# Kernel tuning notes

Hardware: AMD Instinct MI355X
Metric: run time of the kernel (lower is better)

## Reference

```python
import jax, jax.numpy as jnp
import numpy as np

N_NODES = 100000
N_EDGES = 3200000
D_FEAT = 64
CLAMP = 20.0
POSINF = 1.0e6
NEGINF = -1.0e6


def setup_inputs() -> dict:
    key = jax.random.key(0)
    k1, k2, k3, k4 = jax.random.split(key, 4)
    x = jax.random.normal(k1, (N_NODES, D_FEAT), dtype=jnp.float32)
    edge_src = jax.random.randint(k2, (N_EDGES,), 0, N_NODES, dtype=jnp.int64 if jax.config.jax_enable_x64 else jnp.int32).astype(jnp.int32)
    edge_dst = jax.random.randint(k3, (N_EDGES,), 0, N_NODES, dtype=jnp.int32)
    # symmetric-normalized-adjacency-like positive weights
    edge_w = jax.random.uniform(k4, (N_EDGES,), dtype=jnp.float32)
    t = jnp.zeros((1,), dtype=jnp.float32)
    return {"t": t, "x": x, "edge_src": edge_src, "edge_dst": edge_dst, "edge_w": edge_w}


def reference(t, x, edge_src, edge_dst, edge_w):
    # out = sparse.mm(G, x): out[dst] += w * x[src]  (COO SpMM via segment_sum)
    msgs = edge_w[:, None] * x[edge_src]                 # [E, d]
    out = jax.ops.segment_sum(msgs, edge_dst, num_segments=N_NODES)  # [N, d]
    # numerical_stability epilogue: nan/inf sanitize + clamp
    out = jnp.nan_to_num(out, nan=0.0, posinf=POSINF, neginf=NEGINF)
    out = jnp.clip(out, -CLAMP, CLAMP)
    return out
```

## Files before the change

### kernel.cpp

```cpp
#include <hip/hip_runtime.h>
#include <hip/hip_fp16.h>
#include <math.h>

#define N_NODES 100000
#define N_EDGES 3200000
#define D_FEAT  64
#define CLAMP_V 20.0f

#define BSH 6
#define BSZ 64
#define NB  1563
#define SBNSH 11
#define NSB 49
#define FPS 32
#define CPAD 32
#define CHUNKP 4096
#define NCHUNK ((N_EDGES + CHUNKP - 1) / CHUNKP)
#define CH2 4096
#define SLICES 16
#define CAPL 2560
#define HISTB 512
#define NSLC 4
#define NBIN 256


__global__ __launch_bounds__(256)
void prep_kernel(const float4* __restrict__ xin, ushort4* __restrict__ xh,
                 const int* __restrict__ edst, int* __restrict__ counts,
                 int n4) {
    __shared__ int h[NB];
    if (blockIdx.x < HISTB) {
        for (int i = threadIdx.x; i < NB; i += blockDim.x) h[i] = 0;
        __syncthreads();
        const int4* d4p = (const int4*)edst;
        int total4 = N_EDGES >> 2;
        for (int i = blockIdx.x * blockDim.x + threadIdx.x; i < total4;
             i += HISTB * blockDim.x) {
            int4 d4 = d4p[i];
            atomicAdd(&h[d4.x >> BSH], 1);
            atomicAdd(&h[d4.y >> BSH], 1);
            atomicAdd(&h[d4.z >> BSH], 1);
            atomicAdd(&h[d4.w >> BSH], 1);
        }
        __syncthreads();
        for (int i = threadIdx.x; i < NB; i += blockDim.x) {
            int v = h[i];
            if (v) atomicAdd(&counts[i * CPAD], v);
        }
    } else {
        int i = (blockIdx.x - HISTB) * blockDim.x + threadIdx.x;
        if (i < n4) {
            float4 v = xin[i];
            ushort4 o;
            o.x = __half_as_ushort(__float2half(v.x));
            o.y = __half_as_ushort(__float2half(v.y));
            o.z = __half_as_ushort(__float2half(v.z));
            o.w = __half_as_ushort(__float2half(v.w));
            xh[i] = o;
        }
    }
}

__global__ void scan_kernel(const int* __restrict__ counts,
                            int* __restrict__ bstarts,
                            int* __restrict__ cursors2,
                            int* __restrict__ cursors1) {
    __shared__ int wsum[16];
    int t = threadIdx.x;
    int lane = t & 63, wv = t >> 6;
    int b0 = t * 2, b1 = t * 2 + 1;
    int c0 = (b0 < NB) ? counts[b0 * CPAD] : 0;
    int c1 = (b1 < NB) ? counts[b1 * CPAD] : 0;
    int v = c0 + c1;
    int sc = v;
#pragma unroll
    for (int off = 1; off < 64; off <<= 1) {
        int u = __shfl_up(sc, off);
        if (lane >= off) sc += u;
    }
    if (lane == 63) wsum[wv] = sc;
    __syncthreads();
    if (wv == 0 && lane < 16) {
        int ws = wsum[lane];
#pragma unroll
        for (int off = 1; off < 16; off <<= 1) {
            int u = __shfl_up(ws, off);
            if (lane >= off) ws += u;
        }
        wsum[lane] = ws;
    }
    __syncthreads();
    int base = (wv > 0) ? wsum[wv - 1] : 0;
    int incl = base + sc;
    int excl = incl - v;
    if (b0 < NB) { bstarts[b0] = excl;      cursors2[b0 * CPAD] = excl; }
    if (b1 < NB) { bstarts[b1] = excl + c0; cursors2[b1 * CPAD] = excl + c0; }
    if (t == 1023) bstarts[NB] = incl;
    __syncthreads();
    if (t < NSB) cursors1[t * CPAD] = bstarts[t * FPS];
}

__global__ __launch_bounds__(512)
void pass1_kernel(const int* __restrict__ esrc,
                  const int* __restrict__ edst,
                  const float* __restrict__ ew,
                  int* __restrict__ cursors1,
                  unsigned* __restrict__ rk32,
                  unsigned short* __restrict__ ra16) {
    __shared__ unsigned       spk[CHUNKP];
    __shared__ unsigned short sax[CHUNKP];
    __shared__ unsigned char  binof[CHUNKP];
    __shared__ int h[NSB];
    __shared__ int hstart[NSB];
    __shared__ int lcur[NSB];
    __shared__ int lbase[NSB];

    int c0   = blockIdx.x * CHUNKP;
    int cend = min(c0 + CHUNKP, N_EDGES);
    int n    = cend - c0;
    int nv   = n >> 2;
    const int4*   d4p = (const int4*)(edst + c0);
    const int4*   s4p = (const int4*)(esrc + c0);
    const float4* w4p = (const float4*)(ew + c0);
    int t = threadIdx.x;

    if (t < NSB) h[t] = 0;
    __syncthreads();
    for (int i = t; i < nv; i += 512) {
        int4 d4 = d4p[i];
        atomicAdd(&h[d4.x >> SBNSH], 1);
        atomicAdd(&h[d4.y >> SBNSH], 1);
        atomicAdd(&h[d4.z >> SBNSH], 1);
        atomicAdd(&h[d4.w >> SBNSH], 1);
    }
    __syncthreads();
    if (t < NSB) {
        int c = h[t];
        int sc = c;
#pragma unroll
        for (int off = 1; off < 64; off <<= 1) {
            int u = __shfl_up(sc, off);
            if (t >= off) sc += u;
        }
        int excl = sc - c;
        hstart[t] = excl;
        lcur[t]   = excl;
        lbase[t]  = c ? atomicAdd(&cursors1[t * CPAD], c) : 0;
    }
    __syncthreads();
    for (int i = t; i < nv; i += 512) {
        int4   d4 = d4p[i];
        int4   s4 = s4p[i];
        float4 w4 = w4p[i];
#define PUT(dd, ss, ww)                                                       \
        {                                                                     \
            int bk  = (dd) >> SBNSH;                                          \
            int pos = atomicAdd(&lcur[bk], 1);                                \
            unsigned hw = __half_as_ushort(__float2half(ww));                 \
            spk[pos] = ((hw & 0xFFFEu) << 16) | (unsigned)(ss);               \
            sax[pos] = (unsigned short)((dd) & 2047);                         \
            binof[pos] = (unsigned char)bk;                                   \
        }
        PUT(d4.x, s4.x, w4.x);
        PUT(d4.y, s4.y, w4.y);
        PUT(d4.z, s4.z, w4.z);
        PUT(d4.w, s4.w, w4.w);
#undef PUT
    }
    __syncthreads();
    for (int i = t; i < n; i += 512) {
        int bk = binof[i];
        int o  = lbase[bk] + (i - hstart[bk]);
        rk32[o] = spk[i];
        ra16[o] = sax[i];
    }
}

__global__ __launch_bounds__(512)
void pass2_kernel(const unsigned* __restrict__ rk32,
                  const unsigned short* __restrict__ ra16,
                  const int* __restrict__ bstarts,
                  int* __restrict__ cursors2,
                  unsigned* __restrict__ pk32,
                  unsigned char* __restrict__ nd8) {
    __shared__ unsigned      spk[CH2];
    __shared__ unsigned char snd[CH2];
    __shared__ unsigned char binof[CH2];
    __shared__ int h[FPS];
    __shared__ int lstart[FPS];
    __shared__ int lcur[FPS];
    __shared__ int gbase[FPS];

    int sb    = blockIdx.y;
    int f0    = sb * FPS;
    int fend  = min(f0 + FPS, NB);
    int sb0   = bstarts[f0];
    int sbend = bstarts[fend];
    int t = threadIdx.x;

    for (int s = sb0 + blockIdx.x * CH2; s < sbend; s += SLICES * CH2) {
        int n = min(sbend - s, CH2);
        if (t < FPS) h[t] = 0;
        __syncthreads();
        for (int i = t; i < n; i += 512)
            atomicAdd(&h[(ra16[s + i] >> 6) & (FPS - 1)], 1);
        __syncthreads();
        if (t < FPS) {
            int c = h[t];
            int sc = c;
#pragma unroll
            for (int off = 1; off < 32; off <<= 1) {
                int u = __shfl_up(sc, off);
                if (t >= off) sc += u;
            }
            int excl = sc - c;
            lstart[t] = excl;
            lcur[t]   = excl;
            gbase[t]  = (c && f0 + t < NB)
                          ? atomicAdd(&cursors2[(f0 + t) * CPAD], c) : 0;
        }
        __syncthreads();
        for (int i = t; i < n; i += 512) {
            unsigned       pk = rk32[s + i];
            unsigned short ax = ra16[s + i];
            int fk  = (ax >> 6) & (FPS - 1);
            int pos = atomicAdd(&lcur[fk], 1);
            spk[pos] = pk;
            snd[pos] = (unsigned char)(ax & 63u);
            binof[pos] = (unsigned char)fk;
        }
        __syncthreads();
        for (int i = t; i < n; i += 512) {
            int fk = binof[i];
            int o  = gbase[fk] + (i - lstart[fk]);
            pk32[o] = spk[i];
            nd8[o]  = snd[i];
        }
        __syncthreads();
    }
}

__global__ __launch_bounds__(512)
void sort_gather_kernel(const __half* __restrict__ xh,
                        const unsigned* __restrict__ pk32,
                        const unsigned char* __restrict__ nd8,
                        const int* __restrict__ bstarts,
                        float* __restrict__ out) {
    __shared__ unsigned sbuf[CAPL];
    __shared__ int h[NBIN + 1];
    __shared__ int cur[NBIN];
    __shared__ int wsum4[4];
    int t    = threadIdx.x;
    int lane = t & 63;
    int wv   = t >> 6;
    int g    = lane >> 4;
    int s    = lane & 15;
    const char* xbase = (const char*)xh + (s << 3);

    int b   = blockIdx.x;
    int beg = bstarts[b];
    int cnt = bstarts[b + 1] - beg;
    if (cnt > CAPL) cnt = CAPL;

    if (t <= NBIN) h[t] = 0;
    __syncthreads();
    for (int e = t; e < cnt; e += 512) {
        unsigned p = pk32[beg + e];
        int bin = (int)(((p >> 15) & 3u) << 6) | (int)nd8[beg + e];
        atomicAdd(&h[bin + 1], 1);
    }
    __syncthreads();
    if (t < NBIN) {
        int sc = h[t + 1];
#pragma unroll
        for (int off = 1; off < 64; off <<= 1) {
            int u = __shfl_up(sc, off);
            if (lane >= off) sc += u;
        }
        if (lane == 63) wsum4[wv] = sc;
        __syncthreads();
        if (t == 0) {
            int r = 0;
#pragma unroll
            for (int j = 0; j < 4; ++j) { int v = wsum4[j]; wsum4[j] = r; r += v; }
        }
        __syncthreads();
        h[t + 1] = sc + wsum4[wv];
    } else {
        __syncthreads();
        __syncthreads();
    }
    __syncthreads();
    if (t < NBIN) cur[t] = h[t];
    __syncthreads();
    for (int e = t; e < cnt; e += 512) {
        unsigned p = pk32[beg + e];
        int bin = (int)(((p >> 15) & 3u) << 6) | (int)nd8[beg + e];
        sbuf[atomicAdd(&cur[bin], 1)] = p;
    }
    __syncthreads();

#define GSTEP(EE, A0, A1, A2, A3)                                            \
    {                                                                        \
        unsigned p = sbuf[(EE) + g];                                         \
        float wf = __half2float(__ushort_as_half(                            \
                       (unsigned short)((p >> 16) & 0xFFFEu)));              \
        const ushort4 xv = *(const ushort4*)(xbase +                         \
                       ((size_t)((p & 0x1FFFFu) << 7)));                     \
        A0 = fmaf(__half2float(__ushort_as_half(xv.x)), wf, A0);             \
        A1 = fmaf(__half2float(__ushort_as_half(xv.y)), wf, A1);             \
        A2 = fmaf(__half2float(__ushort_as_half(xv.z)), wf, A2);             \
        A3 = fmaf(__half2float(__ushort_as_half(xv.w)), wf, A3);             \
    }
#define GSTEPC(EE, S1, A0, A1, A2, A3)                                       \
    {                                                                        \
        int eg = (EE) + g;                                                   \
        unsigned p = sbuf[eg < (S1) ? eg : ((S1) - 1)];                      \
        float wf = (eg < (S1)) ? __half2float(__ushort_as_half(              \
                       (unsigned short)((p >> 16) & 0xFFFEu))) : 0.0f;       \
        const ushort4 xv = *(const ushort4*)(xbase +                         \
                       ((size_t)((p & 0x1FFFFu) << 7)));                     \
        A0 = fmaf(__half2float(__ushort_as_half(xv.x)), wf, A0);             \
        A1 = fmaf(__half2float(__ushort_as_half(xv.y)), wf, A1);             \
        A2 = fmaf(__half2float(__ushort_as_half(xv.z)), wf, A2);             \
        A3 = fmaf(__half2float(__ushort_as_half(xv.w)), wf, A3);             \
    }

    int node0 = b << BSH;
    float ak0[8], ak1[8], ak2[8], ak3[8];
#pragma unroll
    for (int k = 0; k < 8; ++k) { ak0[k] = 0.f; ak1[k] = 0.f; ak2[k] = 0.f; ak3[k] = 0.f; }
    for (int blk = 0; blk < NSLC; ++blk) {
#pragma unroll
        for (int k = 0; k < 8; ++k) {
            int seg = (blk << 6) | ((wv << 3) + k);
            int s0 = h[seg];
            int s1 = h[seg + 1];
            int e = s0;
            for (; e + 8 <= s1; e += 8) {
                GSTEP(e,     ak0[k], ak1[k], ak2[k], ak3[k]);
                GSTEP(e + 4, ak0[k], ak1[k], ak2[k], ak3[k]);
            }
            for (; e + 4 <= s1; e += 4)
                GSTEP(e, ak0[k], ak1[k], ak2[k], ak3[k]);
            if (e < s1)
                GSTEPC(e, s1, ak0[k], ak1[k], ak2[k], ak3[k]);
        }
    }
#pragma unroll
    for (int k = 0; k < 8; ++k) {
        float a0 = ak0[k], a1 = ak1[k], a2 = ak2[k], a3 = ak3[k];
        a0 += __shfl_xor(a0, 16); a0 += __shfl_xor(a0, 32);
        a1 += __shfl_xor(a1, 16); a1 += __shfl_xor(a1, 32);
        a2 += __shfl_xor(a2, 16); a2 += __shfl_xor(a2, 32);
        a3 += __shfl_xor(a3, 16); a3 += __shfl_xor(a3, 32);
        if (isnan(a0)) a0 = 0.0f;
        if (isnan(a1)) a1 = 0.0f;
        if (isnan(a2)) a2 = 0.0f;
        if (isnan(a3)) a3 = 0.0f;
        a0 = fminf(fmaxf(a0, -CLAMP_V), CLAMP_V);
        a1 = fminf(fmaxf(a1, -CLAMP_V), CLAMP_V);
        a2 = fminf(fmaxf(a2, -CLAMP_V), CLAMP_V);
        a3 = fminf(fmaxf(a3, -CLAMP_V), CLAMP_V);
        int node = node0 + (wv << 3) + k;
        if (lane < 16 && node < N_NODES)
            *(float4*)(out + ((size_t)node << 6) + (s << 2)) =
                make_float4(a0, a1, a2, a3);
    }
#undef GSTEP
#undef GSTEPC
}

__global__ void zero_kernel(float4* __restrict__ out, int n4) {
    int i = blockIdx.x * blockDim.x + threadIdx.x;
    if (i < n4) out[i] = make_float4(0.f, 0.f, 0.f, 0.f);
}

__global__ void scatter_kernel(const float* __restrict__ x,
                               const int* __restrict__ esrc,
                               const int* __restrict__ edst,
                               const float* __restrict__ ew,
                               float* __restrict__ out) {
    long long tid = (long long)blockIdx.x * blockDim.x + threadIdx.x;
    int edge = (int)(tid >> 4);
    int q    = (int)(tid & 15);
    if (edge >= N_EDGES) return;
    int   s = esrc[edge];
    int   d = edst[edge];
    float w = ew[edge];
    const float4* xrow = (const float4*)(x + (size_t)s * D_FEAT);
    float4 v = xrow[q];
    float* orow = out + (size_t)d * D_FEAT + q * 4;
    atomicAdd(orow + 0, w * v.x);
    atomicAdd(orow + 1, w * v.y);
    atomicAdd(orow + 2, w * v.z);
    atomicAdd(orow + 3, w * v.w);
}

__global__ void epilogue_kernel(float4* __restrict__ out, int n4) {
    int i = blockIdx.x * blockDim.x + threadIdx.x;
    if (i >= n4) return;
    float4 v = out[i];
    float* p = &v.x;
#pragma unroll
    for (int k = 0; k < 4; ++k) {
        float f = p[k];
        if (isnan(f)) f = 0.0f;
        f = fminf(fmaxf(f, -CLAMP_V), CLAMP_V);
        p[k] = f;
    }
    out[i] = v;
}

extern "C" void kernel_launch(void* const* d_in, const int* in_sizes, int n_in,
                              void* d_out, int out_size, void* d_ws, size_t ws_size,
                              hipStream_t stream) {
    const float* x    = (const float*)d_in[1];
    const int*   esrc = (const int*)d_in[2];
    const int*   edst = (const int*)d_in[3];
    const float* ew   = (const float*)d_in[4];
    float*       out  = (float*)d_out;

    size_t meta_ints = (size_t)NB * CPAD
                     + (NB + 1)
                     + (size_t)NSB * CPAD
                     + (size_t)NB * CPAD;
    meta_ints = (meta_ints + 1) & ~(size_t)1;
    size_t rk_bytes  = (size_t)N_EDGES * sizeof(unsigned);
    size_t ra_bytes  = (size_t)N_EDGES * sizeof(unsigned short);
    size_t xh_bytes  = (size_t)N_NODES * D_FEAT * sizeof(__half);
    size_t need_alias = meta_ints * sizeof(int) + rk_bytes + ra_bytes
                      + xh_bytes;
    size_t need_full  = need_alias + (size_t)N_EDGES * 5;

    if (ws_size >= need_alias) {
        int*      counts   = (int*)d_ws;
        int*      bstarts  = counts + (size_t)NB * CPAD;
        int*      cursors1 = bstarts + (NB + 1);
        int*      cursors2 = cursors1 + (size_t)NSB * CPAD;
        unsigned* rk32     = (unsigned*)((int*)d_ws + meta_ints);
        unsigned short* ra16 = (unsigned short*)((char*)rk32 + rk_bytes);
        __half*   xh       = (__half*)((char*)ra16 + ra_bytes);

        unsigned*      pk32;
        unsigned char* nd8;
        if (ws_size >= need_full) {
            pk32 = (unsigned*)((char*)xh + xh_bytes);
            nd8  = (unsigned char*)(pk32 + N_EDGES);
        } else {
            pk32 = (unsigned*)edst;
            nd8  = (unsigned char*)ew;
        }

        hipMemsetAsync(counts, 0, (size_t)NB * CPAD * sizeof(int), stream);
        {
            int n4 = N_NODES * D_FEAT / 4;
            prep_kernel<<<HISTB + (n4 + 255) / 256, 256, 0, stream>>>(
                (const float4*)x, (ushort4*)xh, edst, counts, n4);
        }
        scan_kernel<<<1, 1024, 0, stream>>>(counts, bstarts, cursors2, cursors1);
        pass1_kernel<<<NCHUNK, 512, 0, stream>>>(esrc, edst, ew, cursors1,
                                                 rk32, ra16);
        pass2_kernel<<<dim3(SLICES, NSB), 512, 0, stream>>>(rk32, ra16, bstarts,
                                                            cursors2, pk32, nd8);
        sort_gather_kernel<<<NB, 512, 0, stream>>>(xh, pk32, nd8, bstarts, out);
    } else {
        const int n4 = N_NODES * D_FEAT / 4;
        zero_kernel<<<(n4 + 255) / 256, 256, 0, stream>>>((float4*)out, n4);
        long long total = (long long)N_EDGES * 16;
        scatter_kernel<<<(int)((total + 255) / 256), 256, 0, stream>>>(x, esrc, edst, ew, out);
        epilogue_kernel<<<(n4 + 255) / 256, 256, 0, stream>>>((float4*)out, n4);
    }
}
```

Measured before the change: 247.9 us.

## Interleave four segment gathers and stage sort keys in LDS

The gather loop now walks four destination segments at once, issuing four independent feature loads per iteration so more memory requests are in flight per wave. The counting sort keeps each packed edge and its bin in shared memory after the histogram pass, so the scatter pass no longer reloads pk32 and nd8 from global memory. SLICES is also raised from 16 to 32, which affects an earlier kernel. The cost is about 12.8 KB of extra LDS per block, which may lower occupancy, and more unrolled code, which raises register pressure.

```diff
diff --git a/kernel.cpp b/kernel.cpp
--- a/kernel.cpp
+++ b/kernel.cpp
@@ -17,7 +17,7 @@
 #define CHUNKP 4096
 #define NCHUNK ((N_EDGES + CHUNKP - 1) / CHUNKP)
 #define CH2 4096
-#define SLICES 16
+#define SLICES 32
 #define CAPL 2560
 #define HISTB 512
 #define NSLC 4
@@ -246,7 +246,9 @@
                         const unsigned char* __restrict__ nd8,
                         const int* __restrict__ bstarts,
                         float* __restrict__ out) {
-    __shared__ unsigned sbuf[CAPL];
+    __shared__ unsigned      sbuf[CAPL];
+    __shared__ unsigned      stg[CAPL];
+    __shared__ unsigned char sbin[CAPL];
     __shared__ int h[NBIN + 1];
     __shared__ int cur[NBIN];
     __shared__ int wsum4[4];
@@ -267,6 +269,8 @@
     for (int e = t; e < cnt; e += 512) {
         unsigned p = pk32[beg + e];
         int bin = (int)(((p >> 15) & 3u) << 6) | (int)nd8[beg + e];
+        stg[e]  = p;
+        sbin[e] = (unsigned char)bin;
         atomicAdd(&h[bin + 1], 1);
     }
     __syncthreads();
@@ -294,25 +298,25 @@
     if (t < NBIN) cur[t] = h[t];
     __syncthreads();
     for (int e = t; e < cnt; e += 512) {
-        unsigned p = pk32[beg + e];
-        int bin = (int)(((p >> 15) & 3u) << 6) | (int)nd8[beg + e];
+        unsigned p = stg[e];
+        int bin = sbin[e];
         sbuf[atomicAdd(&cur[bin], 1)] = p;
     }
     __syncthreads();
 
-#define GSTEP(EE, A0, A1, A2, A3)                                            \
+#define GS4(EE, K)                                                           \
     {                                                                        \
         unsigned p = sbuf[(EE) + g];                                         \
         float wf = __half2float(__ushort_as_half(                            \
                        (unsigned short)((p >> 16) & 0xFFFEu)));              \
         const ushort4 xv = *(const ushort4*)(xbase +                         \
                        ((size_t)((p & 0x1FFFFu) << 7)));                     \
-        A0 = fmaf(__half2float(__ushort_as_half(xv.x)), wf, A0);             \
-        A1 = fmaf(__half2float(__ushort_as_half(xv.y)), wf, A1);             \
-        A2 = fmaf(__half2float(__ushort_as_half(xv.z)), wf, A2);             \
-        A3 = fmaf(__half2float(__ushort_as_half(xv.w)), wf, A3);             \
-    }
-#define GSTEPC(EE, S1, A0, A1, A2, A3)                                       \
+        ak0[K] = fmaf(__half2float(__ushort_as_half(xv.x)), wf, ak0[K]);     \
+        ak1[K] = fmaf(__half2float(__ushort_as_half(xv.y)), wf, ak1[K]);     \
+        ak2[K] = fmaf(__half2float(__ushort_as_half(xv.z)), wf, ak2[K]);     \
+        ak3[K] = fmaf(__half2float(__ushort_as_half(xv.w)), wf, ak3[K]);     \
+    }
+#define GS4C(EE, S1, K)                                                      \
     {                                                                        \
         int eg = (EE) + g;                                                   \
         unsigned p = sbuf[eg < (S1) ? eg : ((S1) - 1)];                      \
@@ -320,31 +324,47 @@
                        (unsigned short)((p >> 16) & 0xFFFEu))) : 0.0f;       \
         const ushort4 xv = *(const ushort4*)(xbase +                         \
                        ((size_t)((p & 0x1FFFFu) << 7)));                     \
-        A0 = fmaf(__half2float(__ushort_as_half(xv.x)), wf, A0);             \
-        A1 = fmaf(__half2float(__ushort_as_half(xv.y)), wf, A1);             \
-        A2 = fmaf(__half2float(__ushort_as_half(xv.z)), wf, A2);             \
-        A3 = fmaf(__half2float(__ushort_as_half(xv.w)), wf, A3);             \
+        ak0[K] = fmaf(__half2float(__ushort_as_half(xv.x)), wf, ak0[K]);     \
+        ak1[K] = fmaf(__half2float(__ushort_as_half(xv.y)), wf, ak1[K]);     \
+        ak2[K] = fmaf(__half2float(__ushort_as_half(xv.z)), wf, ak2[K]);     \
+        ak3[K] = fmaf(__half2float(__ushort_as_half(xv.w)), wf, ak3[K]);     \
     }
 
     int node0 = b << BSH;
     float ak0[8], ak1[8], ak2[8], ak3[8];
 #pragma unroll
     for (int k = 0; k < 8; ++k) { ak0[k] = 0.f; ak1[k] = 0.f; ak2[k] = 0.f; ak3[k] = 0.f; }
+#pragma unroll 1
     for (int blk = 0; blk < NSLC; ++blk) {
 #pragma unroll
-        for (int k = 0; k < 8; ++k) {
-            int seg = (blk << 6) | ((wv << 3) + k);
-            int s0 = h[seg];
-            int s1 = h[seg + 1];
-            int e = s0;
-            for (; e + 8 <= s1; e += 8) {
-                GSTEP(e,     ak0[k], ak1[k], ak2[k], ak3[k]);
-                GSTEP(e + 4, ak0[k], ak1[k], ak2[k], ak3[k]);
+        for (int kk = 0; kk < 8; kk += 4) {
+            int sb0 = (blk << 6) | (wv << 3) | kk;
+            int hA = h[sb0];
+            int hB = h[sb0 + 1];
+            int hC = h[sb0 + 2];
+            int hD = h[sb0 + 3];
+            int hE = h[sb0 + 4];
+            int eA = hA, eB = hB, eC = hC, eD = hD;
+            while ((eA + 4 <= hB) & (eB + 4 <= hC) &
+                   (eC + 4 <= hD) & (eD + 4 <= hE)) {
+                GS4(eA, kk + 0);
+                GS4(eB, kk + 1);
+                GS4(eC, kk + 2);
+                GS4(eD, kk + 3);
+                eA += 4; eB += 4; eC += 4; eD += 4;
             }
-            for (; e + 4 <= s1; e += 4)
-                GSTEP(e, ak0[k], ak1[k], ak2[k], ak3[k]);
-            if (e < s1)
-                GSTEPC(e, s1, ak0[k], ak1[k], ak2[k], ak3[k]);
+            for (; eA + 8 <= hB; eA += 8) { GS4(eA, kk + 0); GS4(eA + 4, kk + 0); }
+            for (; eA + 4 <= hB; eA += 4) GS4(eA, kk + 0);
+            if (eA < hB) GS4C(eA, hB, kk + 0);
+            for (; eB + 8 <= hC; eB += 8) { GS4(eB, kk + 1); GS4(eB + 4, kk + 1); }
+            for (; eB + 4 <= hC; eB += 4) GS4(eB, kk + 1);
+            if (eB < hC) GS4C(eB, hC, kk + 1);
+            for (; eC + 8 <= hD; eC += 8) { GS4(eC, kk + 2); GS4(eC + 4, kk + 2); }
+            for (; eC + 4 <= hD; eC += 4) GS4(eC, kk + 2);
+            if (eC < hD) GS4C(eC, hD, kk + 2);
+            for (; eD + 8 <= hE; eD += 8) { GS4(eD, kk + 3); GS4(eD + 4, kk + 3); }
+            for (; eD + 4 <= hE; eD += 4) GS4(eD, kk + 3);
+            if (eD < hE) GS4C(eD, hE, kk + 3);
         }
     }
 #pragma unroll
@@ -367,8 +387,8 @@
             *(float4*)(out + ((size_t)node << 6) + (s << 2)) =
                 make_float4(a0, a1, a2, a3);
     }
-#undef GSTEP
-#undef GSTEPC
+#undef GS4
+#undef GS4C
 }
 
 __global__ void zero_kernel(float4* __restrict__ out, int n4) {
```

Result: no change. 251.4 us (+1.4%).

## Drop second partition pass; filter superbucket edges inside gather blocks

Applied to the files above, without the earlier changes.

Removes the second radix-partition kernel and instead has each gather block scan its entire 1024-node superbucket and keep only edges for its 64-node bucket. Superbuckets shrink to 1024 nodes, so the histogram and scan now operate over 98 bins. This saves one kernel launch and one write/read round-trip of the edge stream, but each superbucket is re-read by 16 blocks, which adds filter work and shared atomics.

```diff
diff --git a/kernel.cpp b/kernel.cpp
--- a/kernel.cpp
+++ b/kernel.cpp
@@ -10,14 +10,11 @@
 #define BSH 6
 #define BSZ 64
 #define NB  1563
-#define SBNSH 11
-#define NSB 49
-#define FPS 32
+#define SBNSH 10
+#define NSB 98
 #define CPAD 32
 #define CHUNKP 4096
 #define NCHUNK ((N_EDGES + CHUNKP - 1) / CHUNKP)
-#define CH2 4096
-#define SLICES 16
 #define CAPL 2560
 #define HISTB 512
 #define NSLC 4
@@ -28,24 +25,24 @@
 void prep_kernel(const float4* __restrict__ xin, ushort4* __restrict__ xh,
                  const int* __restrict__ edst, int* __restrict__ counts,
                  int n4) {
-    __shared__ int h[NB];
+    __shared__ int h[NSB];
     if (blockIdx.x < HISTB) {
-        for (int i = threadIdx.x; i < NB; i += blockDim.x) h[i] = 0;
+        if (threadIdx.x < NSB) h[threadIdx.x] = 0;
         __syncthreads();
         const int4* d4p = (const int4*)edst;
         int total4 = N_EDGES >> 2;
         for (int i = blockIdx.x * blockDim.x + threadIdx.x; i < total4;
              i += HISTB * blockDim.x) {
             int4 d4 = d4p[i];
-            atomicAdd(&h[d4.x >> BSH], 1);
-            atomicAdd(&h[d4.y >> BSH], 1);
-            atomicAdd(&h[d4.z >> BSH], 1);
-            atomicAdd(&h[d4.w >> BSH], 1);
-        }
-        __syncthreads();
-        for (int i = threadIdx.x; i < NB; i += blockDim.x) {
-            int v = h[i];
-            if (v) atomicAdd(&counts[i * CPAD], v);
+            atomicAdd(&h[d4.x >> SBNSH], 1);
+            atomicAdd(&h[d4.y >> SBNSH], 1);
+            atomicAdd(&h[d4.z >> SBNSH], 1);
+            atomicAdd(&h[d4.w >> SBNSH], 1);
+        }
+        __syncthreads();
+        if (threadIdx.x < NSB) {
+            int v = h[threadIdx.x];
+            if (v) atomicAdd(&counts[threadIdx.x * CPAD], v);
         }
     } else {
         int i = (blockIdx.x - HISTB) * blockDim.x + threadIdx.x;
@@ -62,42 +59,27 @@
 }
 
 __global__ void scan_kernel(const int* __restrict__ counts,
-                            int* __restrict__ bstarts,
-                            int* __restrict__ cursors2,
+                            int* __restrict__ bstartsSB,
                             int* __restrict__ cursors1) {
-    __shared__ int wsum[16];
+    __shared__ int wtot[2];
     int t = threadIdx.x;
     int lane = t & 63, wv = t >> 6;
-    int b0 = t * 2, b1 = t * 2 + 1;
-    int c0 = (b0 < NB) ? counts[b0 * CPAD] : 0;
-    int c1 = (b1 < NB) ? counts[b1 * CPAD] : 0;
-    int v = c0 + c1;
-    int sc = v;
+    int c = (t < NSB) ? counts[t * CPAD] : 0;
+    int sc = c;
 #pragma unroll
     for (int off = 1; off < 64; off <<= 1) {
         int u = __shfl_up(sc, off);
         if (lane >= off) sc += u;
     }
-    if (lane == 63) wsum[wv] = sc;
-    __syncthreads();
-    if (wv == 0 && lane < 16) {
-        int ws = wsum[lane];
-#pragma unroll
-        for (int off = 1; off < 16; off <<= 1) {
-            int u = __shfl_up(ws, off);
-            if (lane >= off) ws += u;
-        }
-        wsum[lane] = ws;
-    }
-    __syncthreads();
-    int base = (wv > 0) ? wsum[wv - 1] : 0;
-    int incl = base + sc;
-    int excl = incl - v;
-    if (b0 < NB) { bstarts[b0] = excl;      cursors2[b0 * CPAD] = excl; }
-    if (b1 < NB) { bstarts[b1] = excl + c0; cursors2[b1 * CPAD] = excl + c0; }
-    if (t == 1023) bstarts[NB] = incl;
-    __syncthreads();
-    if (t < NSB) cursors1[t * CPAD] = bstarts[t * FPS];
+    if (lane == 63) wtot[wv] = sc;
+    __syncthreads();
+    int base = (wv == 1) ? wtot[0] : 0;
+    int excl = base + sc - c;
+    if (t < NSB) {
+        bstartsSB[t] = excl;
+        cursors1[t * CPAD] = excl;
+    }
+    if (t == 0) bstartsSB[NSB] = N_EDGES;
 }
 
 __global__ __launch_bounds__(512)
@@ -114,6 +96,7 @@
     __shared__ int hstart[NSB];
     __shared__ int lcur[NSB];
     __shared__ int lbase[NSB];
+    __shared__ int wtot[2];
 
     int c0   = blockIdx.x * CHUNKP;
     int cend = min(c0 + CHUNKP, N_EDGES);
@@ -134,15 +117,21 @@
         atomicAdd(&h[d4.w >> SBNSH], 1);
     }
     __syncthreads();
-    if (t < NSB) {
-        int c = h[t];
-        int sc = c;
+    int c = 0, sc = 0;
+    if (t < 128) {
+        c = (t < NSB) ? h[t] : 0;
+        sc = c;
 #pragma unroll
         for (int off = 1; off < 64; off <<= 1) {
             int u = __shfl_up(sc, off);
-            if (t >= off) sc += u;
-        }
-        int excl = sc - c;
+            if ((t & 63) >= off) sc += u;
+        }
+        if ((t & 63) == 63) wtot[t >> 6] = sc;
+    }
+    __syncthreads();
+    if (t < NSB) {
+        int base = (t >= 64) ? wtot[0] : 0;
+        int excl = base + sc - c;
         hstart[t] = excl;
         lcur[t]   = excl;
         lbase[t]  = c ? atomicAdd(&cursors1[t * CPAD], c) : 0;
@@ -158,7 +147,7 @@
             int pos = atomicAdd(&lcur[bk], 1);                                \
             unsigned hw = __half_as_ushort(__float2half(ww));                 \
             spk[pos] = ((hw & 0xFFFEu) << 16) | (unsigned)(ss);               \
-            sax[pos] = (unsigned short)((dd) & 2047);                         \
+            sax[pos] = (unsigned short)((dd) & 1023);                         \
             binof[pos] = (unsigned char)bk;                                   \
         }
         PUT(d4.x, s4.x, w4.x);
@@ -177,79 +166,18 @@
 }
 
 __global__ __launch_bounds__(512)
-void pass2_kernel(const unsigned* __restrict__ rk32,
-                  const unsigned short* __restrict__ ra16,
-                  const int* __restrict__ bstarts,
-                  int* __restrict__ cursors2,
-                  unsigned* __restrict__ pk32,
-                  unsigned char* __restrict__ nd8) {
-    __shared__ unsigned      spk[CH2];
-    __shared__ unsigned char snd[CH2];
-    __shared__ unsigned char binof[CH2];
-    __shared__ int h[FPS];
-    __shared__ int lstart[FPS];
-    __shared__ int lcur[FPS];
-    __shared__ int gbase[FPS];
-
-    int sb    = blockIdx.y;
-    int f0    = sb * FPS;
-    int fend  = min(f0 + FPS, NB);
-    int sb0   = bstarts[f0];
-    int sbend = bstarts[fend];
-    int t = threadIdx.x;
-
-    for (int s = sb0 + blockIdx.x * CH2; s < sbend; s += SLICES * CH2) {
-        int n = min(sbend - s, CH2);
-        if (t < FPS) h[t] = 0;
-        __syncthreads();
-        for (int i = t; i < n; i += 512)
-            atomicAdd(&h[(ra16[s + i] >> 6) & (FPS - 1)], 1);
-        __syncthreads();
-        if (t < FPS) {
-            int c = h[t];
-            int sc = c;
-#pragma unroll
-            for (int off = 1; off < 32; off <<= 1) {
-                int u = __shfl_up(sc, off);
-                if (t >= off) sc += u;
-            }
-            int excl = sc - c;
-            lstart[t] = excl;
-            lcur[t]   = excl;
-            gbase[t]  = (c && f0 + t < NB)
-                          ? atomicAdd(&cursors2[(f0 + t) * CPAD], c) : 0;
-        }
-        __syncthreads();
-        for (int i = t; i < n; i += 512) {
-            unsigned       pk = rk32[s + i];
-            unsigned short ax = ra16[s + i];
-            int fk  = (ax >> 6) & (FPS - 1);
-            int pos = atomicAdd(&lcur[fk], 1);
-            spk[pos] = pk;
-            snd[pos] = (unsigned char)(ax & 63u);
-            binof[pos] = (unsigned char)fk;
-        }
-        __syncthreads();
-        for (int i = t; i < n; i += 512) {
-            int fk = binof[i];
-            int o  = gbase[fk] + (i - lstart[fk]);
-            pk32[o] = spk[i];
-            nd8[o]  = snd[i];
-        }
-        __syncthreads();
-    }
-}
-
-__global__ __launch_bounds__(512)
 void sort_gather_kernel(const __half* __restrict__ xh,
-                        const unsigned* __restrict__ pk32,
-                        const unsigned char* __restrict__ nd8,
-                        const int* __restrict__ bstarts,
+                        const unsigned* __restrict__ rk32,
+                        const unsigned short* __restrict__ ra16,
+                        const int* __restrict__ bstartsSB,
                         float* __restrict__ out) {
-    __shared__ unsigned sbuf[CAPL];
+    __shared__ unsigned      sbuf[CAPL];
+    __shared__ unsigned      stg[CAPL];
+    __shared__ unsigned char sbin[CAPL];
     __shared__ int h[NBIN + 1];
     __shared__ int cur[NBIN];
     __shared__ int wsum4[4];
+    __shared__ int mcnt;
     int t    = threadIdx.x;
     int lane = t & 63;
     int wv   = t >> 6;
@@ -257,19 +185,42 @@
     int s    = lane & 15;
     const char* xbase = (const char*)xh + (s << 3);
 
-    int b   = blockIdx.x;
-    int beg = bstarts[b];
-    int cnt = bstarts[b + 1] - beg;
+    int b    = blockIdx.x;
+    int sbid = b >> 4;
+    int fk   = b & 15;
+    int sbeg = bstartsSB[sbid];
+    int send = bstartsSB[sbid + 1];
+
+    if (t <= NBIN) h[t] = 0;
+    if (t == 0) mcnt = 0;
+    __syncthreads();
+    int a0 = sbeg & ~3;
+    for (int i0 = a0 + t * 4; i0 < send; i0 += 512 * 4) {
+        int4    r4 = *(const int4*)(rk32 + i0);
+        ushort4 a4 = *(const ushort4*)(ra16 + i0);
+#define FILT(J, RR, AA)                                                       \
+        {                                                                     \
+            int idx = i0 + (J);                                               \
+            if (idx >= sbeg && idx < send && (int)((AA) >> 6) == fk) {        \
+                int bin = (int)((((unsigned)(RR) >> 15) & 3u) << 6)           \
+                        | (int)((AA) & 63u);                                  \
+                int pos = atomicAdd(&mcnt, 1);                                \
+                if (pos < CAPL) {                                             \
+                    stg[pos]  = (unsigned)(RR);                               \
+                    sbin[pos] = (unsigned char)bin;                           \
+                    atomicAdd(&h[bin + 1], 1);                                \
+                }                                                             \
+            }                                                                 \
+        }
+        FILT(0, r4.x, a4.x);
+        FILT(1, r4.y, a4.y);
+        FILT(2, r4.z, a4.z);
+        FILT(3, r4.w, a4.w);
+#undef FILT
+    }
+    __syncthreads();
+    int cnt = mcnt;
     if (cnt > CAPL) cnt = CAPL;
-
-    if (t <= NBIN) h[t] = 0;
-    __syncthreads();
-    for (int e = t; e < cnt; e += 512) {
-        unsigned p = pk32[beg + e];
-        int bin = (int)(((p >> 15) & 3u) << 6) | (int)nd8[beg + e];
-        atomicAdd(&h[bin + 1], 1);
-    }
-    __syncthreads();
     if (t < NBIN) {
         int sc = h[t + 1];
 #pragma unroll
@@ -294,25 +245,23 @@
     if (t < NBIN) cur[t] = h[t];
     __syncthreads();
     for (int e = t; e < cnt; e += 512) {
-        unsigned p = pk32[beg + e];
-        int bin = (int)(((p >> 15) & 3u) << 6) | (int)nd8[beg + e];
-        sbuf[atomicAdd(&cur[bin], 1)] = p;
-    }
-    __syncthreads();
-
-#define GSTEP(EE, A0, A1, A2, A3)                                            \
+        sbuf[atomicAdd(&cur[sbin[e]], 1)] = stg[e];
+    }
+    __syncthreads();
+
+#define GSTEP(EE, K)                                                         \
     {                                                                        \
         unsigned p = sbuf[(EE) + g];                                         \
         float wf = __half2float(__ushort_as_half(                            \
                        (unsigned short)((p >> 16) & 0xFFFEu)));              \
         const ushort4 xv = *(const ushort4*)(xbase +                         \
                        ((size_t)((p & 0x1FFFFu) << 7)));                     \
-        A0 = fmaf(__half2float(__ushort_as_half(xv.x)), wf, A0);             \
-        A1 = fmaf(__half2float(__ushort_as_half(xv.y)), wf, A1);             \
-        A2 = fmaf(__half2float(__ushort_as_half(xv.z)), wf, A2);             \
-        A3 = fmaf(__half2float(__ushort_as_half(xv.w)), wf, A3);             \
-    }
-#define GSTEPC(EE, S1, A0, A1, A2, A3)                                       \
+        ak0[K] = fmaf(__half2float(__ushort_as_half(xv.x)), wf, ak0[K]);     \
+        ak1[K] = fmaf(__half2float(__ushort_as_half(xv.y)), wf, ak1[K]);     \
+        ak2[K] = fmaf(__half2float(__ushort_as_half(xv.z)), wf, ak2[K]);     \
+        ak3[K] = fmaf(__half2float(__ushort_as_half(xv.w)), wf, ak3[K]);     \
+    }
+#define GSTEPC(EE, S1, K)                                                    \
     {                                                                        \
         int eg = (EE) + g;                                                   \
         unsigned p = sbuf[eg < (S1) ? eg : ((S1) - 1)];                      \
@@ -320,16 +269,17 @@
                        (unsigned short)((p >> 16) & 0xFFFEu))) : 0.0f;       \
         const ushort4 xv = *(const ushort4*)(xbase +                         \
                        ((size_t)((p & 0x1FFFFu) << 7)));                     \
-        A0 = fmaf(__half2float(__ushort_as_half(xv.x)), wf, A0);             \
-        A1 = fmaf(__half2float(__ushort_as_half(xv.y)), wf, A1);             \
-        A2 = fmaf(__half2float(__ushort_as_half(xv.z)), wf, A2);             \
-        A3 = fmaf(__half2float(__ushort_as_half(xv.w)), wf, A3);             \
+        ak0[K] = fmaf(__half2float(__ushort_as_half(xv.x)), wf, ak0[K]);     \
+        ak1[K] = fmaf(__half2float(__ushort_as_half(xv.y)), wf, ak1[K]);     \
+        ak2[K] = fmaf(__half2float(__ushort_as_half(xv.z)), wf, ak2[K]);     \
+        ak3[K] = fmaf(__half2float(__ushort_as_half(xv.w)), wf, ak3[K]);     \
     }
 
     int node0 = b << BSH;
     float ak0[8], ak1[8], ak2[8], ak3[8];
 #pragma unroll
     for (int k = 0; k < 8; ++k) { ak0[k] = 0.f; ak1[k] = 0.f; ak2[k] = 0.f; ak3[k] = 0.f; }
+#pragma unroll 1
     for (int blk = 0; blk < NSLC; ++blk) {
 #pragma unroll
         for (int k = 0; k < 8; ++k) {
@@ -338,13 +288,13 @@
             int s1 = h[seg + 1];
             int e = s0;
             for (; e + 8 <= s1; e += 8) {
-                GSTEP(e,     ak0[k], ak1[k], ak2[k], ak3[k]);
-                GSTEP(e + 4, ak0[k], ak1[k], ak2[k], ak3[k]);
+                GSTEP(e, k);
+                GSTEP(e + 4, k);
             }
             for (; e + 4 <= s1; e += 4)
-                GSTEP(e, ak0[k], ak1[k], ak2[k], ak3[k]);
+                GSTEP(e, k);
             if (e < s1)
-                GSTEPC(e, s1, ak0[k], ak1[k], ak2[k], ak3[k]);
+                GSTEPC(e, s1, k);
         }
     }
 #pragma unroll
@@ -421,49 +371,34 @@
     const float* ew   = (const float*)d_in[4];
     float*       out  = (float*)d_out;
 
-    size_t meta_ints = (size_t)NB * CPAD
-                     + (NB + 1)
-                     + (size_t)NSB * CPAD
-                     + (size_t)NB * CPAD;
-    meta_ints = (meta_ints + 1) & ~(size_t)1;
+    size_t meta_ints = (size_t)NSB * CPAD
+                     + (NSB + 1)
+                     + (size_t)NSB * CPAD;
+    meta_ints = (meta_ints + 3) & ~(size_t)3;
     size_t rk_bytes  = (size_t)N_EDGES * sizeof(unsigned);
     size_t ra_bytes  = (size_t)N_EDGES * sizeof(unsigned short);
     size_t xh_bytes  = (size_t)N_NODES * D_FEAT * sizeof(__half);
-    size_t need_alias = meta_ints * sizeof(int) + rk_bytes + ra_bytes
-                      + xh_bytes;
-    size_t need_full  = need_alias + (size_t)N_EDGES * 5;
-
-    if (ws_size >= need_alias) {
-        int*      counts   = (int*)d_ws;
-        int*      bstarts  = counts + (size_t)NB * CPAD;
-        int*      cursors1 = bstarts + (NB + 1);
-        int*      cursors2 = cursors1 + (size_t)NSB * CPAD;
-        unsigned* rk32     = (unsigned*)((int*)d_ws + meta_ints);
+    size_t need = meta_ints * sizeof(int) + rk_bytes + ra_bytes + xh_bytes;
+
+    if (ws_size >= need) {
+        int*      counts    = (int*)d_ws;
+        int*      bstartsSB = counts + (size_t)NSB * CPAD;
+        int*      cursors1  = bstartsSB + (NSB + 1);
+        unsigned* rk32      = (unsigned*)((int*)d_ws + meta_ints);
         unsigned short* ra16 = (unsigned short*)((char*)rk32 + rk_bytes);
-        __half*   xh       = (__half*)((char*)ra16 + ra_bytes);
-
-        unsigned*      pk32;
-        unsigned char* nd8;
-        if (ws_size >= need_full) {
-            pk32 = (unsigned*)((char*)xh + xh_bytes);
-            nd8  = (unsigned char*)(pk32 + N_EDGES);
-        } else {
-            pk32 = (unsigned*)edst;
-            nd8  = (unsigned char*)ew;
-        }
-
-        hipMemsetAsync(counts, 0, (size_t)NB * CPAD * sizeof(int), stream);
+        __half*   xh        = (__half*)((char*)ra16 + ra_bytes);
+
+        hipMemsetAsync(counts, 0, (size_t)NSB * CPAD * sizeof(int), stream);
         {
             int n4 = N_NODES * D_FEAT / 4;
             prep_kernel<<<HISTB + (n4 + 255) / 256, 256, 0, stream>>>(
                 (const float4*)x, (ushort4*)xh, edst, counts, n4);
         }
-        scan_kernel<<<1, 1024, 0, stream>>>(counts, bstarts, cursors2, cursors1);
+        scan_kernel<<<1, 128, 0, stream>>>(counts, bstartsSB, cursors1);
         pass1_kernel<<<NCHUNK, 512, 0, stream>>>(esrc, edst, ew, cursors1,
                                                  rk32, ra16);
-        pass2_kernel<<<dim3(SLICES, NSB), 512, 0, stream>>>(rk32, ra16, bstarts,
-                                                            cursors2, pk32, nd8);
-        sort_gather_kernel<<<NB, 512, 0, stream>>>(xh, pk32, nd8, bstarts, out);
+        sort_gather_kernel<<<NB, 512, 0, stream>>>(xh, rk32, ra16, bstartsSB,
+                                                   out);
     } else {
         const int n4 = N_NODES * D_FEAT / 4;
         zero_kernel<<<(n4 + 255) / 256, 256, 0, stream>>>((float4*)out, n4);
```

New measurement: 238.5 us. 1.04x faster.
